# Kernel tuning notes

Measured on AMD Instinct MI355X. Metric: run time of the kernel, lower is better.

The kernel has to match this reference:

```python
import jax, jax.numpy as jnp
import numpy as np

N_NODES = 100000


def setup_inputs() -> dict:
    key = jax.random.key(0)
    ks = jax.random.split(key, 4)
    x = jax.random.normal(ks[0], (N_NODES, 64), dtype=jnp.float32)
    edge_index = jax.random.randint(ks[1], (2, 1600000), 0, N_NODES, dtype=jnp.int64)
    # Glorot-ish scaled weights
    W1 = jax.random.normal(ks[2], (64, 64), dtype=jnp.float32) * (1.0 / np.sqrt(64))
    b1 = jnp.zeros((64,), dtype=jnp.float32)
    W2 = jax.random.normal(ks[3], (64, 19), dtype=jnp.float32) * (1.0 / np.sqrt(64))
    b2 = jnp.zeros((19,), dtype=jnp.float32)
    return {"x": x, "edge_index": edge_index, "W1": W1, "b1": b1, "W2": W2, "b2": b2}


def _gcn_norm(edge_index, num_nodes, dtype):
    # PyG gcn_norm: add self-loops (fill_value=1, improved=False), then
    # norm = deg^-1/2[src] * deg^-1/2[dst] with deg computed over destination.
    loops = jnp.arange(num_nodes, dtype=edge_index.dtype)
    src = jnp.concatenate([edge_index[0], loops])
    dst = jnp.concatenate([edge_index[1], loops])
    deg = jax.ops.segment_sum(jnp.ones_like(dst, dtype=dtype), dst, num_segments=num_nodes)
    dinv = jax.lax.rsqrt(deg)  # deg >= 1 thanks to self-loops
    norm = dinv[src] * dinv[dst]  # [E + N]
    return src, dst, norm


def _gcn_conv(h, src, dst, norm, W, b, num_nodes):
    hw = h @ W                                  # dense transform [N, d_out]
    msg = norm[:, None] * hw[src]               # gather + edge scaling [E+N, d_out]
    out = jax.ops.segment_sum(msg, dst, num_segments=num_nodes)  # scatter-add
    return out + b


def reference(x, edge_index, W1, b1, W2, b2):
    n = x.shape[0]
    src, dst, norm = _gcn_norm(edge_index, n, x.dtype)
    h = jax.nn.relu(_gcn_conv(x, src, dst, norm, W1, b1, n))
    # dropout is identity in eval mode (training=False)
    return _gcn_conv(h, src, dst, norm, W2, b2, n)
```

## Files before the change

### kernel.cpp

```cpp
#include <hip/hip_runtime.h>

#define TPB 256
#define BSH 5
#define BNODES 32
#define CAP 1024
#define EPB 4096
#define NBMAX 3200


__global__ void k_hist1(const int* __restrict__ dst, int* __restrict__ hist,
                        int nb, int E) {
    __shared__ int sh[NBMAX];
    int tid = threadIdx.x, blk = blockIdx.x;
    for (int i = tid; i < nb; i += TPB) sh[i] = 0;
    __syncthreads();
    int e0 = blk * EPB;
    for (int i = tid; i < EPB; i += TPB) {
        int e = e0 + i;
        if (e < E) atomicAdd(&sh[dst[e] >> BSH], 1);
    }
    __syncthreads();
    int* hrow = hist + (size_t)blk * nb;
    for (int i = tid; i < nb; i += TPB) hrow[i] = sh[i];
}

__global__ void k_scanoff(const int* __restrict__ hist, int* __restrict__ offs,
                          int* __restrict__ bcnt, int nblk, int nb) {
    int t = blockIdx.x * TPB + threadIdx.x;
    int b = t >> 3, s = t & 7;
    if (b >= nb) return;
    int nps = (nblk + 7) >> 3;
    int sum = 0;
    for (int q = 0; q < nps; ++q) {
        int blk = q * 8 + s;
        if (blk < nblk) sum += hist[(size_t)blk * nb + b];
    }
    int v = sum;
#pragma unroll
    for (int o = 1; o < 8; o <<= 1) {
        int u = __shfl_up(v, o, 8);
        if (s >= o) v += u;
    }
    int total = __shfl(v, 7, 8);
    if (s == 0) bcnt[b] = total;
    int off = b * CAP + (v - sum);
    for (int q = 0; q < nps; ++q) {
        int blk = q * 8 + s;
        if (blk < nblk) {
            offs[(size_t)blk * nb + b] = off;
            off += hist[(size_t)blk * nb + b];
        }
    }
}

__global__ void k_scatter(const int* __restrict__ src, const int* __restrict__ dst,
                          const int* __restrict__ offs, unsigned* __restrict__ ebuf,
                          int nb, int E) {
    __shared__ int cur[NBMAX];
    int tid = threadIdx.x, blk = blockIdx.x;
    const int* orow = offs + (size_t)blk * nb;
    for (int i = tid; i < nb; i += TPB) cur[i] = orow[i];
    __syncthreads();
    int e0 = blk * EPB;
    for (int i = tid; i < EPB; i += TPB) {
        int e = e0 + i;
        if (e < E) {
            int d = dst[e];
            int pos = atomicAdd(&cur[d >> BSH], 1);
            ebuf[pos] = ((unsigned)src[e] << BSH) | (unsigned)(d & (BNODES - 1));
        }
    }
}

__global__ void k_bcsr(const int* __restrict__ bcnt, const unsigned* __restrict__ ebuf,
                       int* __restrict__ csr, int* __restrict__ node_beg,
                       int* __restrict__ degi, float* __restrict__ dinv, int nb, int n) {
    __shared__ unsigned se[4][CAP];
    __shared__ int scnt[4][BNODES];
    __shared__ int sexc[4][BNODES];
    __shared__ int srnk[4][BNODES];
    int wv = threadIdx.x >> 6, lane = threadIdx.x & 63;
    int b = blockIdx.x * 4 + wv;
    bool act = (b < nb);
    if (lane < BNODES) { scnt[wv][lane] = 0; srnk[wv][lane] = 0; }
    __syncthreads();
    int cnt = 0;
    if (act) {
        cnt = bcnt[b];
        if (cnt > CAP) cnt = CAP;
        const unsigned* p = &ebuf[(size_t)b * CAP];
        for (int k = lane; k < cnt; k += 64) {
            unsigned pk = p[k];
            se[wv][k] = pk;
            atomicAdd(&scnt[wv][pk & (BNODES - 1)], 1);
        }
    }
    __syncthreads();
    if (act && lane < BNODES) {
        int dg = scnt[wv][lane];
        int v = dg;
#pragma unroll
        for (int off = 1; off < BNODES; off <<= 1) {
            int t = __shfl_up(v, off, BNODES);
            if (lane >= off) v += t;
        }
        int excl = v - dg;
        sexc[wv][lane] = excl;
        int node = b * BNODES + lane;
        if (node < n) {
            degi[node] = dg;
            node_beg[node] = b * CAP + excl;
            dinv[node] = rsqrtf((float)dg + 1.0f);
        }
    }
    __syncthreads();
    if (act) {
        int* csrb = csr + (size_t)b * CAP;
        for (int k = lane; k < cnt; k += 64) {
            unsigned pk = se[wv][k];
            int dl = pk & (BNODES - 1);
            int r = atomicAdd(&srnk[wv][dl], 1);
            csrb[sexc[wv][dl] + r] = (int)(pk >> BSH);
        }
    }
}


__global__ void k_xw64s(const float* __restrict__ x, const float* __restrict__ W,
                        const float* __restrict__ dinv, _Float16* __restrict__ g, int n) {
    __shared__ float Ws[64 * 64];
    __shared__ float xs[4][64];
    int tid = threadIdx.x;
    for (int i = tid; i < 64 * 64; i += TPB) Ws[i] = W[i];
    int r = tid >> 6, c = tid & 63;
    int row = blockIdx.x * 4 + r;
    if (row < n) xs[r][c] = x[(size_t)row * 64 + c];
    __syncthreads();
    if (row < n) {
        float acc = 0.f;
#pragma unroll
        for (int k = 0; k < 64; ++k) acc += xs[r][k] * Ws[k * 64 + c];
        g[(size_t)row * 64 + c] = (_Float16)(dinv[row] * acc);
    }
}

__global__ void k_xw19s(const _Float16* __restrict__ h, const float* __restrict__ W,
                        const float* __restrict__ dinv, _Float16* __restrict__ g2, int n) {
    __shared__ float Ws[64][20];
    __shared__ float xs[8][64];
    int tid = threadIdx.x;
    for (int i = tid; i < 64 * 19; i += TPB) Ws[i / 19][i % 19] = W[i];
    for (int i = tid; i < 8 * 64; i += TPB) {
        int rr = i >> 6, cc = i & 63;
        int row = blockIdx.x * 8 + rr;
        if (row < n) xs[rr][cc] = (float)h[(size_t)row * 64 + cc];
    }
    __syncthreads();
    int r = tid >> 5, c = tid & 31;
    int row = blockIdx.x * 8 + r;
    if (row < n && c < 19) {
        float acc = 0.f;
#pragma unroll
        for (int k = 0; k < 64; ++k) acc += xs[r][k] * Ws[k][c];
        g2[(size_t)row * 19 + c] = (_Float16)(dinv[row] * acc);
    }
}


__global__ void k_gather64(const int* __restrict__ node_beg, const int* __restrict__ degi,
                           const int* __restrict__ csr, const float* __restrict__ dinv,
                           const _Float16* __restrict__ g, const float* __restrict__ b1,
                           _Float16* __restrict__ h, int n) {
    int node = blockIdx.x * 4 + (threadIdx.x >> 6);
    if (node >= n) return;
    int lane = threadIdx.x & 63;
    int eidx = lane >> 3, fch = lane & 7;
    int beg = node_beg[node], cnt = degi[node];
    float acc[8];
#pragma unroll
    for (int j = 0; j < 8; ++j) acc[j] = 0.f;
    for (int base = 0; base < cnt; base += 8) {
        int k = base + eidx;
        if (k < cnt) {
            int row = csr[beg + k];
            uint4 v = *((const uint4*)(g + (size_t)row * 64) + fch);
            const _Float16* f = (const _Float16*)&v;
#pragma unroll
            for (int j = 0; j < 8; ++j) acc[j] += (float)f[j];
        }
    }
#pragma unroll
    for (int m = 8; m < 64; m <<= 1) {
#pragma unroll
        for (int j = 0; j < 8; ++j) acc[j] += __shfl_xor(acc[j], m);
    }
    if (eidx == 0) {
        uint4 v = *((const uint4*)(g + (size_t)node * 64) + fch);
        const _Float16* f = (const _Float16*)&v;
        float dv = dinv[node];
        _Float16 outv[8];
#pragma unroll
        for (int j = 0; j < 8; ++j) {
            float val = dv * (acc[j] + (float)f[j]) + b1[fch * 8 + j];
            outv[j] = (_Float16)fmaxf(val, 0.f);
        }
        *((uint4*)(h + (size_t)node * 64) + fch) = *(const uint4*)outv;
    }
}

__global__ void k_gather19(const int* __restrict__ node_beg, const int* __restrict__ degi,
                           const int* __restrict__ csr, const float* __restrict__ dinv,
                           const _Float16* __restrict__ g2, const float* __restrict__ b2,
                           float* __restrict__ out, int n) {
    int node = blockIdx.x * 8 + (threadIdx.x >> 5);
    if (node >= n) return;
    int c = threadIdx.x & 31;
    if (c >= 19) return;
    int beg = node_beg[node], cnt = degi[node];
    float a0 = (float)g2[(size_t)node * 19 + c];
    float a1 = 0.f, a2 = 0.f, a3 = 0.f;
    int k = 0;
    for (; k + 3 < cnt; k += 4) {
        int s0 = csr[beg + k];
        int s1 = csr[beg + k + 1];
        int s2 = csr[beg + k + 2];
        int s3 = csr[beg + k + 3];
        a0 += (float)g2[(size_t)s0 * 19 + c];
        a1 += (float)g2[(size_t)s1 * 19 + c];
        a2 += (float)g2[(size_t)s2 * 19 + c];
        a3 += (float)g2[(size_t)s3 * 19 + c];
    }
    for (; k < cnt; ++k) a1 += (float)g2[(size_t)csr[beg + k] * 19 + c];
    out[(size_t)node * 19 + c] = dinv[node] * ((a0 + a1) + (a2 + a3)) + b2[c];
}


extern "C" void kernel_launch(void* const* d_in, const int* in_sizes, int n_in,
                              void* d_out, int out_size, void* d_ws, size_t ws_size,
                              hipStream_t stream) {
    const float* x  = (const float*)d_in[0];
    const int*   ei = (const int*)d_in[1];
    const float* W1 = (const float*)d_in[2];
    const float* b1 = (const float*)d_in[3];
    const float* W2 = (const float*)d_in[4];
    const float* b2 = (const float*)d_in[5];
    float* out = (float*)d_out;

    int N = in_sizes[0] / 64;
    int E = in_sizes[1] / 2;
    const int* src = ei;
    const int* dst = ei + E;

    int NB = (N + BNODES - 1) >> BSH;
    int NBLK = (E + EPB - 1) / EPB;

    char* w = (char*)d_ws;
    int* bcnt      = (int*)w;      w += (size_t)NB * 4;
    int* degi      = (int*)w;      w += (size_t)N * 4;
    int* node_beg  = (int*)w;      w += (size_t)N * 4;
    float* dinv    = (float*)w;    w += (size_t)N * 4;
    w = (char*)(((size_t)w + 63) & ~(size_t)63);
    char* regionA  = w;
    size_t histB   = (size_t)NBLK * NB * 4;
    size_t csrB    = (size_t)NB * CAP * 4;
    size_t regA    = (histB * 2 > csrB) ? histB * 2 : csrB;
    int* hist      = (int*)regionA;
    int* offs      = (int*)(regionA + histB);
    int* csr       = (int*)regionA;
    w += regA;
    unsigned* ebuf = (unsigned*)w; w += (size_t)NB * CAP * 4;
    _Float16* g1   = (_Float16*)w; w += (size_t)N * 64 * 2;
    _Float16* h    = (_Float16*)w; w += (size_t)N * 64 * 2;
    _Float16* g2   = g1;

    k_hist1   <<<NBLK, TPB, 0, stream>>>(dst, hist, NB, E);
    k_scanoff <<<(NB * 8 + TPB - 1) / TPB, TPB, 0, stream>>>(hist, offs, bcnt, NBLK, NB);
    k_scatter <<<NBLK, TPB, 0, stream>>>(src, dst, offs, ebuf, NB, E);
    k_bcsr    <<<(NB + 3) / 4, TPB, 0, stream>>>(bcnt, ebuf, csr, node_beg, degi, dinv, NB, N);

    k_xw64s   <<<(N + 3) / 4, TPB, 0, stream>>>(x, W1, dinv, g1, N);
    k_gather64<<<(N + 3) / 4, TPB, 0, stream>>>(node_beg, degi, csr, dinv, g1, b1, h, N);

    k_xw19s   <<<(N + 7) / 8, TPB, 0, stream>>>(h, W2, dinv, g2, N);
    k_gather19<<<(N + 7) / 8, TPB, 0, stream>>>(node_beg, degi, csr, dinv, g2, b2, out, N);
}
```

Measured before the change: 230.9 us.

## Register-tile dense transforms and pad layer-2 features to 32 for vectorized gather

The 64x64 transform now handles 64 rows per block, stages x transposed in shared memory and accumulates a 4x4 register tile per thread, which cuts shared-memory traffic and amortizes the weight load. The 64x19 transform writes a zero-padded 32-wide fp16 layout. The second-layer gather uses that layout to read 16-byte vectors, with 16 edges in parallel per wavefront and a shuffle reduction, replacing scalar 2-byte strided loads. Padding raises the g2 memory footprint and the larger blocks use more shared memory per block.

```diff
diff --git a/kernel.cpp b/kernel.cpp
--- a/kernel.cpp
+++ b/kernel.cpp
@@ -126,43 +126,95 @@
 }
 
 
-__global__ void k_xw64s(const float* __restrict__ x, const float* __restrict__ W,
+__global__ void k_xw64v(const float* __restrict__ x, const float* __restrict__ W,
                         const float* __restrict__ dinv, _Float16* __restrict__ g, int n) {
     __shared__ float Ws[64 * 64];
-    __shared__ float xs[4][64];
+    __shared__ float xsT[64 * 64];
     int tid = threadIdx.x;
-    for (int i = tid; i < 64 * 64; i += TPB) Ws[i] = W[i];
-    int r = tid >> 6, c = tid & 63;
-    int row = blockIdx.x * 4 + r;
-    if (row < n) xs[r][c] = x[(size_t)row * 64 + c];
-    __syncthreads();
-    if (row < n) {
-        float acc = 0.f;
-#pragma unroll
-        for (int k = 0; k < 64; ++k) acc += xs[r][k] * Ws[k * 64 + c];
-        g[(size_t)row * 64 + c] = (_Float16)(dinv[row] * acc);
-    }
-}
-
-__global__ void k_xw19s(const _Float16* __restrict__ h, const float* __restrict__ W,
-                        const float* __restrict__ dinv, _Float16* __restrict__ g2, int n) {
-    __shared__ float Ws[64][20];
-    __shared__ float xs[8][64];
+    int row0 = blockIdx.x * 64;
+    for (int i = tid; i < 1024; i += TPB)
+        reinterpret_cast<float4*>(Ws)[i] = reinterpret_cast<const float4*>(W)[i];
+    {
+        int rl = tid >> 2, cq = (tid & 3) * 16;
+        int row = row0 + rl;
+#pragma unroll
+        for (int j4 = 0; j4 < 4; ++j4) {
+            float4 v = make_float4(0.f, 0.f, 0.f, 0.f);
+            if (row < n) v = *reinterpret_cast<const float4*>(x + (size_t)row * 64 + cq + j4 * 4);
+            xsT[(cq + j4 * 4 + 0) * 64 + rl] = v.x;
+            xsT[(cq + j4 * 4 + 1) * 64 + rl] = v.y;
+            xsT[(cq + j4 * 4 + 2) * 64 + rl] = v.z;
+            xsT[(cq + j4 * 4 + 3) * 64 + rl] = v.w;
+        }
+    }
+    __syncthreads();
+    int c4 = (tid & 15) * 4, rq = (tid >> 4) * 4;
+    float acc[4][4] = {};
+#pragma unroll 4
+    for (int k = 0; k < 64; ++k) {
+        float4 wv = *reinterpret_cast<const float4*>(Ws + k * 64 + c4);
+        float4 xv = *reinterpret_cast<const float4*>(xsT + k * 64 + rq);
+        const float* wp = (const float*)&wv;
+        const float* xp = (const float*)&xv;
+#pragma unroll
+        for (int i = 0; i < 4; ++i)
+#pragma unroll
+            for (int j = 0; j < 4; ++j) acc[i][j] += xp[i] * wp[j];
+    }
+#pragma unroll
+    for (int i = 0; i < 4; ++i) {
+        int row = row0 + rq + i;
+        if (row < n) {
+            float dv = dinv[row];
+            _Float16 o[4];
+#pragma unroll
+            for (int j = 0; j < 4; ++j) o[j] = (_Float16)(dv * acc[i][j]);
+            *reinterpret_cast<ushort4*>(g + (size_t)row * 64 + c4) =
+                *reinterpret_cast<const ushort4*>(o);
+        }
+    }
+}
+
+__global__ void k_xw19v(const _Float16* __restrict__ h, const float* __restrict__ W,
+                        const float* __restrict__ dinv, _Float16* __restrict__ g2p, int n) {
+    __shared__ float Ws[64 * 32];
+    __shared__ float xsT[64 * 32];
     int tid = threadIdx.x;
-    for (int i = tid; i < 64 * 19; i += TPB) Ws[i / 19][i % 19] = W[i];
-    for (int i = tid; i < 8 * 64; i += TPB) {
-        int rr = i >> 6, cc = i & 63;
-        int row = blockIdx.x * 8 + rr;
-        if (row < n) xs[rr][cc] = (float)h[(size_t)row * 64 + cc];
-    }
-    __syncthreads();
-    int r = tid >> 5, c = tid & 31;
-    int row = blockIdx.x * 8 + r;
-    if (row < n && c < 19) {
-        float acc = 0.f;
-#pragma unroll
-        for (int k = 0; k < 64; ++k) acc += xs[r][k] * Ws[k][c];
-        g2[(size_t)row * 19 + c] = (_Float16)(dinv[row] * acc);
+    int row0 = blockIdx.x * 32;
+    for (int i = tid; i < 64 * 32; i += TPB) {
+        int k = i >> 5, c = i & 31;
+        Ws[i] = (c < 19) ? W[k * 19 + c] : 0.f;
+    }
+    {
+        int rl = tid >> 3, sq = tid & 7;
+        int row = row0 + rl;
+        if (row < n) {
+            uint4 v = *(reinterpret_cast<const uint4*>(h + (size_t)row * 64) + sq);
+            const _Float16* f = (const _Float16*)&v;
+#pragma unroll
+            for (int j = 0; j < 8; ++j) xsT[(sq * 8 + j) * 32 + rl] = (float)f[j];
+        } else {
+#pragma unroll
+            for (int j = 0; j < 8; ++j) xsT[(sq * 8 + j) * 32 + rl] = 0.f;
+        }
+    }
+    __syncthreads();
+    int c = tid & 31, rg = (tid >> 5) * 4;
+    float acc[4] = {};
+#pragma unroll 4
+    for (int k = 0; k < 64; ++k) {
+        float wv = Ws[k * 32 + c];
+        float4 xv = *reinterpret_cast<const float4*>(xsT + k * 32 + rg);
+        const float* xp = (const float*)&xv;
+#pragma unroll
+        for (int i = 0; i < 4; ++i) acc[i] += xp[i] * wv;
+    }
+#pragma unroll
+    for (int i = 0; i < 4; ++i) {
+        int row = row0 + rg + i;
+        if (row < n)
+            g2p[(size_t)row * 32 + c] = (c < 19) ? (_Float16)(dinv[row] * acc[i])
+                                                 : (_Float16)0.f;
     }
 }
 
@@ -208,30 +260,47 @@
     }
 }
 
-__global__ void k_gather19(const int* __restrict__ node_beg, const int* __restrict__ degi,
-                           const int* __restrict__ csr, const float* __restrict__ dinv,
-                           const _Float16* __restrict__ g2, const float* __restrict__ b2,
-                           float* __restrict__ out, int n) {
-    int node = blockIdx.x * 8 + (threadIdx.x >> 5);
+__global__ void k_gath19(const int* __restrict__ node_beg, const int* __restrict__ degi,
+                         const int* __restrict__ csr, const float* __restrict__ dinv,
+                         const _Float16* __restrict__ g2p, const float* __restrict__ b2,
+                         float* __restrict__ out, int n) {
+    int node = blockIdx.x * 4 + (threadIdx.x >> 6);
     if (node >= n) return;
-    int c = threadIdx.x & 31;
-    if (c >= 19) return;
+    int lane = threadIdx.x & 63;
+    int eidx = lane >> 2, fq = lane & 3;
     int beg = node_beg[node], cnt = degi[node];
-    float a0 = (float)g2[(size_t)node * 19 + c];
-    float a1 = 0.f, a2 = 0.f, a3 = 0.f;
-    int k = 0;
-    for (; k + 3 < cnt; k += 4) {
-        int s0 = csr[beg + k];
-        int s1 = csr[beg + k + 1];
-        int s2 = csr[beg + k + 2];
-        int s3 = csr[beg + k + 3];
-        a0 += (float)g2[(size_t)s0 * 19 + c];
-        a1 += (float)g2[(size_t)s1 * 19 + c];
-        a2 += (float)g2[(size_t)s2 * 19 + c];
-        a3 += (float)g2[(size_t)s3 * 19 + c];
-    }
-    for (; k < cnt; ++k) a1 += (float)g2[(size_t)csr[beg + k] * 19 + c];
-    out[(size_t)node * 19 + c] = dinv[node] * ((a0 + a1) + (a2 + a3)) + b2[c];
+    float acc[8];
+#pragma unroll
+    for (int j = 0; j < 8; ++j) acc[j] = 0.f;
+    for (int base = 0; base < cnt; base += 16) {
+        int k = base + eidx;
+        if (k < cnt) {
+            int row = csr[beg + k];
+            uint4 v = *((const uint4*)(g2p + (size_t)row * 32) + fq);
+            const _Float16* f = (const _Float16*)&v;
+#pragma unroll
+            for (int j = 0; j < 8; ++j) acc[j] += (float)f[j];
+        }
+    }
+    if (eidx == 0) {
+        uint4 v = *((const uint4*)(g2p + (size_t)node * 32) + fq);
+        const _Float16* f = (const _Float16*)&v;
+#pragma unroll
+        for (int j = 0; j < 8; ++j) acc[j] += (float)f[j];
+    }
+#pragma unroll
+    for (int m = 4; m < 64; m <<= 1) {
+#pragma unroll
+        for (int j = 0; j < 8; ++j) acc[j] += __shfl_xor(acc[j], m);
+    }
+    if (eidx == 0) {
+        float dv = dinv[node];
+#pragma unroll
+        for (int j = 0; j < 8; ++j) {
+            int cc = fq * 8 + j;
+            if (cc < 19) out[(size_t)node * 19 + cc] = dv * acc[j] + b2[cc];
+        }
+    }
 }
 
 
@@ -271,16 +340,16 @@
     unsigned* ebuf = (unsigned*)w; w += (size_t)NB * CAP * 4;
     _Float16* g1   = (_Float16*)w; w += (size_t)N * 64 * 2;
     _Float16* h    = (_Float16*)w; w += (size_t)N * 64 * 2;
-    _Float16* g2   = g1;
+    _Float16* g2p  = g1;
 
     k_hist1   <<<NBLK, TPB, 0, stream>>>(dst, hist, NB, E);
     k_scanoff <<<(NB * 8 + TPB - 1) / TPB, TPB, 0, stream>>>(hist, offs, bcnt, NBLK, NB);
     k_scatter <<<NBLK, TPB, 0, stream>>>(src, dst, offs, ebuf, NB, E);
     k_bcsr    <<<(NB + 3) / 4, TPB, 0, stream>>>(bcnt, ebuf, csr, node_beg, degi, dinv, NB, N);
 
-    k_xw64s   <<<(N + 3) / 4, TPB, 0, stream>>>(x, W1, dinv, g1, N);
+    k_xw64v   <<<(N + 63) / 64, TPB, 0, stream>>>(x, W1, dinv, g1, N);
     k_gather64<<<(N + 3) / 4, TPB, 0, stream>>>(node_beg, degi, csr, dinv, g1, b1, h, N);
 
-    k_xw19s   <<<(N + 7) / 8, TPB, 0, stream>>>(h, W2, dinv, g2, N);
-    k_gather19<<<(N + 7) / 8, TPB, 0, stream>>>(node_beg, degi, csr, dinv, g2, b2, out, N);
-}
+    k_xw19v   <<<(N + 31) / 32, TPB, 0, stream>>>(h, W2, dinv, g2p, N);
+    k_gath19  <<<(N + 3) / 4, TPB, 0, stream>>>(node_beg, degi, csr, dinv, g2p, b2, out, N);
+}
```

Result: faster. 223.9 us (-3.0%).
